# Optimization experiments

Hardware: AMD Instinct MI355X
Metric: run time of the kernel (lower is better)

## Reference

```python
import jax, jax.numpy as jnp
import numpy as np

D_MODEL = 2048
N_HEADS = 16
HEAD_DIM = D_MODEL // N_HEADS  # 128


def setup_inputs() -> dict:
    key = jax.random.key(0)
    ks = jax.random.split(key, 7)
    B, S, CACHE = 2, 2048, 2048
    scale = 1.0 / np.sqrt(D_MODEL)
    return {
        "x": jax.random.normal(ks[0], (B, S, D_MODEL), dtype=jnp.float32),
        "cached_k": jax.random.normal(ks[1], (B, N_HEADS, CACHE, HEAD_DIM), dtype=jnp.float32),
        "cached_v": jax.random.normal(ks[2], (B, N_HEADS, CACHE, HEAD_DIM), dtype=jnp.float32),
        "W_q": jax.random.normal(ks[3], (D_MODEL, D_MODEL), dtype=jnp.float32) * scale,
        "W_k": jax.random.normal(ks[4], (D_MODEL, D_MODEL), dtype=jnp.float32) * scale,
        "W_v": jax.random.normal(ks[5], (D_MODEL, D_MODEL), dtype=jnp.float32) * scale,
        "W_o": jax.random.normal(ks[6], (D_MODEL, D_MODEL), dtype=jnp.float32) * scale,
    }


def reference(x, cached_k, cached_v, W_q, W_k, W_v, W_o):
    B, S, _ = x.shape
    # nn.Linear(d,d,bias=False): y = x @ W.T
    def proj(W):
        h = jnp.einsum("bsd,ed->bse", x, W)
        return h.reshape(B, S, N_HEADS, HEAD_DIM).transpose(0, 2, 1, 3)  # (B,H,S,Dh)
    q = proj(W_q)
    k = jnp.concatenate([cached_k, proj(W_k)], axis=2)  # (B,H,T,Dh)
    v = jnp.concatenate([cached_v, proj(W_v)], axis=2)
    scores = jnp.einsum("bhsd,bhtd->bhst", q, k) / np.sqrt(HEAD_DIM)
    attn = jax.nn.softmax(scores, axis=-1)
    out = jnp.einsum("bhst,bhtd->bhsd", attn, v)  # (B,H,S,Dh)
    out = out.transpose(0, 2, 1, 3).reshape(B, S, D_MODEL)
    out = jnp.einsum("bsd,ed->bse", out, W_o)
    return out, k, v
```

## Files before the change

### kernel.cpp

```cpp
#include <hip/hip_runtime.h>

typedef __bf16 bf16;
typedef __bf16 bf16x4 __attribute__((ext_vector_type(4)));
typedef __bf16 bf16x8 __attribute__((ext_vector_type(8)));
typedef float f32x4 __attribute__((ext_vector_type(4)));

#define LOG2E 1.44269504088896340736f
#define QSCALE 0.12751884935f
#define RESCALE_THR 8.0f

__device__ __forceinline__ void gload_lds16(const void* gp, void* lp) {
    __builtin_amdgcn_global_load_lds(
        (__attribute__((address_space(1))) void*)gp,
        (__attribute__((address_space(3))) void*)lp,
        16, 0, 0);
}

__device__ __forceinline__ int swz(int j, int row) {
    return (j & 8) | ((j ^ row) & 7);
}

template <int CTRL>
__device__ __forceinline__ float dpp_mov(float x) {
    return __int_as_float(__builtin_amdgcn_update_dpp(
        0, __float_as_int(x), CTRL, 0xF, 0xF, true));
}
__device__ __forceinline__ float rowmax16(float v) {
    v = fmaxf(v, dpp_mov<0x121>(v));
    v = fmaxf(v, dpp_mov<0x122>(v));
    v = fmaxf(v, dpp_mov<0x124>(v));
    v = fmaxf(v, dpp_mov<0x128>(v));
    return v;
}
__device__ __forceinline__ float rowsum16(float v) {
    v += dpp_mov<0x121>(v);
    v += dpp_mov<0x122>(v);
    v += dpp_mov<0x124>(v);
    v += dpp_mov<0x128>(v);
    return v;
}

__global__ void conv_bf16(const float* __restrict__ in, bf16* __restrict__ out, int n4) {
    int i = blockIdx.x * 256 + threadIdx.x;
    if (i < n4) {
        float4 f = ((const float4*)in)[i];
        bf16x4 v;
        v[0] = (bf16)f.x; v[1] = (bf16)f.y; v[2] = (bf16)f.z; v[3] = (bf16)f.w;
        *(bf16x4*)(out + (size_t)i * 4) = v;
    }
}

__global__ void copy_cache_k(const float* __restrict__ ck, float* __restrict__ kout,
                             bf16* __restrict__ kb) {
    size_t i = ((size_t)blockIdx.x * 256 + threadIdx.x) * 4;
    size_t bh  = i >> 18;
    size_t rem = i & 262143;
    size_t o   = (bh << 19) + rem;
    float4 f = *(const float4*)(ck + i);
    *(float4*)(kout + o) = f;
    bf16x4 v;
    v[0] = (bf16)f.x; v[1] = (bf16)f.y; v[2] = (bf16)f.z; v[3] = (bf16)f.w;
    *(bf16x4*)(kb + o) = v;
}

__global__ void copy_cache_v(const float* __restrict__ cv, float* __restrict__ vout,
                             bf16* __restrict__ vtb) {
    __shared__ float tile[32][33];
    int bh = blockIdx.z;
    int t0 = blockIdx.x * 32;
    int dh0 = blockIdx.y * 32;
    int tx = threadIdx.x, ty = threadIdx.y;
    const float* src = cv + (size_t)bh * 2048 * 128;
    float* dstf = vout + (size_t)bh * 4096 * 128;
    #pragma unroll
    for (int i = 0; i < 4; ++i) {
        int t = t0 + ty * 4 + i;
        float val = src[(size_t)t * 128 + dh0 + tx];
        dstf[(size_t)t * 128 + dh0 + tx] = val;
        tile[ty * 4 + i][tx] = val;
    }
    __syncthreads();
    bf16* dstb = vtb + (size_t)bh * 128 * 4096;
    #pragma unroll
    for (int i = 0; i < 4; ++i) {
        int dh = dh0 + ty * 4 + i;
        dstb[(size_t)dh * 4096 + t0 + tx] = (bf16)tile[tx][ty * 4 + i];
    }
}

template <int MODE>
__global__ __launch_bounds__(256)
void gemm_nt(const bf16* __restrict__ A, const bf16* __restrict__ Bm,
             float* __restrict__ out_f32, bf16* __restrict__ out_bf16) {
    const int K = 2048, N = 2048;
    __shared__ __align__(16) char smem[32768];
    const int tid = threadIdx.x;
    const int wid = tid >> 6;
    const int lane = tid & 63;
    const int quad = lane >> 4;
    const int l16 = lane & 15;
    const int m0 = blockIdx.y * 128;
    const int n0 = blockIdx.x * 128;
    const int wm = (wid & 1) * 64;
    const int wn = (wid >> 1) * 64;

    f32x4 zero = {0.f, 0.f, 0.f, 0.f};
    f32x4 acc[4][4];
    #pragma unroll
    for (int i = 0; i < 4; ++i)
        #pragma unroll
        for (int j = 0; j < 4; ++j) acc[i][j] = zero;

    auto stage = [&](int k0, int buf) {
        char* base = smem + buf * 16384;
        #pragma unroll
        for (int t = 0; t < 2; ++t) {
            int c = t * 256 + tid;
            int row = c >> 2, kc = c & 3;
            const char* gA = (const char*)(A + (size_t)(m0 + row) * K + k0 + kc * 8);
            const char* gB = (const char*)(Bm + (size_t)(n0 + row) * K + k0 + kc * 8);
            char* lA = base + (size_t)(t * 256 + (tid & ~63)) * 16;
            char* lB = base + 8192 + (size_t)(t * 256 + (tid & ~63)) * 16;
            gload_lds16(gA, lA);
            gload_lds16(gB, lB);
        }
    };

    stage(0, 0);
    __syncthreads();

    for (int k0 = 0; k0 < K; k0 += 32) {
        const int cur = (k0 >> 5) & 1;
        if (k0 + 32 < K) stage(k0 + 32, cur ^ 1);
        const char* base = smem + cur * 16384;
        bf16x8 af[4], bfv[4];
        #pragma unroll
        for (int i = 0; i < 4; ++i) {
            af[i]  = *(const bf16x8*)(base + ((wm + i * 16 + l16) * 32 + quad * 8) * 2);
            bfv[i] = *(const bf16x8*)(base + 8192 + ((wn + i * 16 + l16) * 32 + quad * 8) * 2);
        }
        __builtin_amdgcn_s_setprio(1);
        #pragma unroll
        for (int i = 0; i < 4; ++i)
            #pragma unroll
            for (int j = 0; j < 4; ++j)
                acc[i][j] = __builtin_amdgcn_mfma_f32_16x16x32_bf16(af[i], bfv[j], acc[i][j], 0, 0, 0);
        __builtin_amdgcn_s_setprio(0);
        __syncthreads();
    }

    #pragma unroll
    for (int i = 0; i < 4; ++i)
        #pragma unroll
        for (int j = 0; j < 4; ++j)
            #pragma unroll
            for (int r = 0; r < 4; ++r) {
                int grow = m0 + wm + i * 16 + quad * 4 + r;
                int gcol = n0 + wn + j * 16 + l16;
                float v = acc[i][j][r];
                if (MODE == 0) {
                    out_f32[(size_t)grow * N + gcol] = v;
                } else {
                    int b = grow >> 11, s = grow & 2047;
                    int h = gcol >> 7, dh = gcol & 127;
                    if (MODE == 1) {
                        out_bf16[(((size_t)(b * 16 + h) * 2048) + s) * 128 + dh] = (bf16)(v * QSCALE);
                    } else if (MODE == 2) {
                        size_t idx = (((size_t)(b * 16 + h) * 4096) + 2048 + s) * 128 + dh;
                        out_f32[idx] = v;
                        out_bf16[idx] = (bf16)v;
                    } else {
                        size_t idx = (((size_t)(b * 16 + h) * 4096) + 2048 + s) * 128 + dh;
                        out_f32[idx] = v;
                        out_bf16[(((size_t)(b * 16 + h) * 128) + dh) * 4096 + 2048 + s] = (bf16)v;
                    }
                }
            }
}

__global__ __launch_bounds__(256, 2)
void flash_attn(const bf16* __restrict__ qb, const bf16* __restrict__ kb,
                const bf16* __restrict__ vtb, bf16* __restrict__ ab) {
    __shared__ __align__(16) char smem[74240];
    const int tid = threadIdx.x;
    const int wid = tid >> 6;
    const int lane = tid & 63;
    const int quad = lane >> 4;
    const int l16 = lane & 15;

    const int flat = blockIdx.x;
    const int xcd = flat & 7;
    const int idx = flat >> 3;
    const int bh = xcd * 4 + (idx >> 4);
    const int qblk = idx & 15;
    const int b = bh >> 4, h = bh & 15;
    const int s0 = qblk * 128 + wid * 32;

    const bf16* Q  = qb  + (size_t)bh * 2048 * 128;
    const bf16* Kp = kb  + (size_t)bh * 4096 * 128;
    const bf16* Vt = vtb + (size_t)bh * 128 * 4096;

    bf16x8 qf[2][4];
    #pragma unroll
    for (int qi = 0; qi < 2; ++qi)
        #pragma unroll
        for (int ks = 0; ks < 4; ++ks)
            qf[qi][ks] = *(const bf16x8*)(Q + (size_t)(s0 + qi * 16 + l16) * 128 + ks * 32 + quad * 8);

    f32x4 zero = {0.f, 0.f, 0.f, 0.f};
    f32x4 oacc[2][8];
    float mrun[2][4], lrun[2][4];
    #pragma unroll
    for (int qi = 0; qi < 2; ++qi) {
        #pragma unroll
        for (int i = 0; i < 8; ++i) oacc[qi][i] = zero;
        #pragma unroll
        for (int r = 0; r < 4; ++r) { mrun[qi][r] = -1e30f; lrun[qi][r] = 0.f; }
    }

    auto stage = [&](int t0, int buf) {
        char* Kb = smem + buf * 32768;
        char* Vb = Kb + 16384;
        #pragma unroll
        for (int r = 0; r < 4; ++r) {
            int kc = r * 256 + tid;
            int row = kc >> 4, p = kc & 15;
            int j = swz(p, row);
            gload_lds16(Kp + (size_t)(t0 + row) * 128 + j * 8, Kb + kc * 16);
        }
        #pragma unroll
        for (int r = 0; r < 4; ++r) {
            int vc = r * 256 + tid;
            int row = vc >> 3, p = vc & 7;
            int j = (p ^ row) & 7;
            gload_lds16(Vt + (size_t)row * 4096 + t0 + j * 8, Vb + vc * 16);
        }
    };

    stage(0, 0);
    __syncthreads();

    for (int t0 = 0; t0 < 4096; t0 += 64) {
        const int cur = (t0 >> 6) & 1;
        if (t0 + 64 < 4096) stage(t0 + 64, cur ^ 1);
        const char* Ksh = smem + cur * 32768;
        const char* Vsh = Ksh + 16384;

        f32x4 sacc[2][4];
        #pragma unroll
        for (int qi = 0; qi < 2; ++qi)
            #pragma unroll
            for (int nt = 0; nt < 4; ++nt) sacc[qi][nt] = zero;
        __builtin_amdgcn_s_setprio(1);
        #pragma unroll
        for (int nt = 0; nt < 4; ++nt) {
            #pragma unroll
            for (int ks = 0; ks < 4; ++ks) {
                bf16x8 kf = *(const bf16x8*)(Ksh + (nt * 16 + l16) * 256 + swz(ks * 4 + quad, l16) * 16);
                sacc[0][nt] = __builtin_amdgcn_mfma_f32_16x16x32_bf16(qf[0][ks], kf, sacc[0][nt], 0, 0, 0);
                sacc[1][nt] = __builtin_amdgcn_mfma_f32_16x16x32_bf16(qf[1][ks], kf, sacc[1][nt], 0, 0, 0);
            }
        }
        __builtin_amdgcn_s_setprio(0);

        bf16x8 pf[2][2];
        char* pb = smem + 65536 + wid * 2176;
        #pragma unroll
        for (int qi = 0; qi < 2; ++qi) {
            float mx[4];
            #pragma unroll
            for (int r = 0; r < 4; ++r) {
                float v0 = fmaxf(fmaxf(sacc[qi][0][r], sacc[qi][1][r]),
                                 fmaxf(sacc[qi][2][r], sacc[qi][3][r]));
                mx[r] = rowmax16(v0);
            }
            bool defer = true;
            #pragma unroll
            for (int r = 0; r < 4; ++r)
                defer = defer && (mx[r] <= mrun[qi][r] + RESCALE_THR);
            if (__all(defer)) {
                float rsum[4] = {0.f, 0.f, 0.f, 0.f};
                #pragma unroll
                for (int nt = 0; nt < 4; ++nt)
                    #pragma unroll
                    for (int r = 0; r < 4; ++r) {
                        float p = __builtin_amdgcn_exp2f(sacc[qi][nt][r] - mrun[qi][r]);
                        sacc[qi][nt][r] = p;
                        rsum[r] += p;
                    }
                #pragma unroll
                for (int r = 0; r < 4; ++r) lrun[qi][r] += rowsum16(rsum[r]);
            } else {
                float alpha[4], mnew[4], rsum[4];
                #pragma unroll
                for (int r = 0; r < 4; ++r) {
                    mnew[r] = fmaxf(mrun[qi][r], mx[r]);
                    alpha[r] = __builtin_amdgcn_exp2f(mrun[qi][r] - mnew[r]);
                    rsum[r] = 0.f;
                }
                #pragma unroll
                for (int nt = 0; nt < 4; ++nt)
                    #pragma unroll
                    for (int r = 0; r < 4; ++r) {
                        float p = __builtin_amdgcn_exp2f(sacc[qi][nt][r] - mnew[r]);
                        sacc[qi][nt][r] = p;
                        rsum[r] += p;
                    }
                #pragma unroll
                for (int r = 0; r < 4; ++r) {
                    lrun[qi][r] = lrun[qi][r] * alpha[r] + rowsum16(rsum[r]);
                    mrun[qi][r] = mnew[r];
                }
                #pragma unroll
                for (int i = 0; i < 8; ++i)
                    #pragma unroll
                    for (int r = 0; r < 4; ++r) oacc[qi][i][r] *= alpha[r];
            }

            #pragma unroll
            for (int nt = 0; nt < 4; ++nt)
                #pragma unroll
                for (int r = 0; r < 4; ++r) {
                    int row = quad * 4 + r;
                    *(bf16*)(pb + row * 136 + nt * 32 + l16 * 2) = (bf16)sacc[qi][nt][r];
                }
            #pragma unroll
            for (int ks = 0; ks < 2; ++ks)
                pf[qi][ks] = *(const bf16x8*)(pb + l16 * 136 + (ks * 4 + quad) * 16);
        }

        __builtin_amdgcn_s_setprio(1);
        #pragma unroll
        for (int dht = 0; dht < 8; ++dht) {
            #pragma unroll
            for (int ks = 0; ks < 2; ++ks) {
                bf16x8 vf = *(const bf16x8*)(Vsh + (dht * 16 + l16) * 128 + swz(ks * 4 + quad, l16) * 16);
                oacc[0][dht] = __builtin_amdgcn_mfma_f32_16x16x32_bf16(pf[0][ks], vf, oacc[0][dht], 0, 0, 0);
                oacc[1][dht] = __builtin_amdgcn_mfma_f32_16x16x32_bf16(pf[1][ks], vf, oacc[1][dht], 0, 0, 0);
            }
        }
        __builtin_amdgcn_s_setprio(0);

        __syncthreads();
    }

    #pragma unroll
    for (int qi = 0; qi < 2; ++qi)
        #pragma unroll
        for (int dht = 0; dht < 8; ++dht)
            #pragma unroll
            for (int r = 0; r < 4; ++r) {
                int s = s0 + qi * 16 + quad * 4 + r;
                float v = oacc[qi][dht][r] / lrun[qi][r];
                ab[((size_t)(b * 2048 + s)) * 2048 + h * 128 + dht * 16 + l16] = (bf16)v;
            }
}

extern "C" void kernel_launch(void* const* d_in, const int* in_sizes, int n_in,
                              void* d_out, int out_size, void* d_ws, size_t ws_size,
                              hipStream_t stream) {
    const float* x        = (const float*)d_in[0];
    const float* cached_k = (const float*)d_in[1];
    const float* cached_v = (const float*)d_in[2];
    const float* W_q      = (const float*)d_in[3];
    const float* W_k      = (const float*)d_in[4];
    const float* W_v      = (const float*)d_in[5];
    const float* W_o      = (const float*)d_in[6];

    float* out  = (float*)d_out;
    float* kout = out + 8388608;
    float* vout = out + 25165824;

    char* ws = (char*)d_ws;
    size_t off = 0;
    auto alloc = [&](size_t elts) { bf16* p = (bf16*)(ws + off); off += elts * 2; return p; };
    bf16* xb  = alloc(8388608);
    bf16* wqb = alloc(4194304);
    bf16* wkb = alloc(4194304);
    bf16* wvb = alloc(4194304);
    bf16* wob = alloc(4194304);
    bf16* qb  = alloc(8388608);
    bf16* kb  = alloc(16777216);
    bf16* vtb = alloc(16777216);
    bf16* ab  = alloc(8388608);

    conv_bf16<<<8192, 256, 0, stream>>>(x, xb, 2097152);
    conv_bf16<<<4096, 256, 0, stream>>>(W_q, wqb, 1048576);
    conv_bf16<<<4096, 256, 0, stream>>>(W_k, wkb, 1048576);
    conv_bf16<<<4096, 256, 0, stream>>>(W_v, wvb, 1048576);
    conv_bf16<<<4096, 256, 0, stream>>>(W_o, wob, 1048576);
    copy_cache_k<<<8192, 256, 0, stream>>>(cached_k, kout, kb);
    copy_cache_v<<<dim3(64, 4, 32), dim3(32, 8), 0, stream>>>(cached_v, vout, vtb);

    gemm_nt<1><<<dim3(16, 32), 256, 0, stream>>>(xb, wqb, nullptr, qb);
    gemm_nt<2><<<dim3(16, 32), 256, 0, stream>>>(xb, wkb, kout, kb);
    gemm_nt<3><<<dim3(16, 32), 256, 0, stream>>>(xb, wvb, vout, vtb);

    flash_attn<<<512, 256, 0, stream>>>(qb, kb, vtb, ab);

    gemm_nt<0><<<dim3(16, 32), 256, 0, stream>>>(ab, wob, out, nullptr);
}
```

Baseline: 733.0 us.

## Restructure flash attention to transposed 32x32x16 MFMA with register-resident P

```diff
diff --git a/kernel.cpp b/kernel.cpp
--- a/kernel.cpp
+++ b/kernel.cpp
@@ -4,6 +4,8 @@
 typedef __bf16 bf16x4 __attribute__((ext_vector_type(4)));
 typedef __bf16 bf16x8 __attribute__((ext_vector_type(8)));
 typedef float f32x4 __attribute__((ext_vector_type(4)));
+typedef float f32x16 __attribute__((ext_vector_type(16)));
+typedef int iv2 __attribute__((ext_vector_type(2)));
 
 #define LOG2E 1.44269504088896340736f
 #define QSCALE 0.12751884935f
@@ -20,24 +22,38 @@
     return (j & 8) | ((j ^ row) & 7);
 }
 
-template <int CTRL>
-__device__ __forceinline__ float dpp_mov(float x) {
-    return __int_as_float(__builtin_amdgcn_update_dpp(
-        0, __float_as_int(x), CTRL, 0xF, 0xF, true));
-}
-__device__ __forceinline__ float rowmax16(float v) {
-    v = fmaxf(v, dpp_mov<0x121>(v));
-    v = fmaxf(v, dpp_mov<0x122>(v));
-    v = fmaxf(v, dpp_mov<0x124>(v));
-    v = fmaxf(v, dpp_mov<0x128>(v));
-    return v;
-}
-__device__ __forceinline__ float rowsum16(float v) {
-    v += dpp_mov<0x121>(v);
-    v += dpp_mov<0x122>(v);
-    v += dpp_mov<0x124>(v);
-    v += dpp_mov<0x128>(v);
-    return v;
+__device__ __forceinline__ unsigned cvtpk(float lo, float hi) {
+    unsigned w;
+    asm("v_cvt_pk_bf16_f32 %0, %1, %2" : "=v"(w) : "v"(lo), "v"(hi));
+    return w;
+}
+
+__device__ __forceinline__ iv2 permswap(unsigned a, unsigned b) {
+    return __builtin_amdgcn_permlane32_swap((int)a, (int)b, false, false);
+}
+__device__ __forceinline__ float halfmax(float v) {
+    iv2 r = permswap(__float_as_uint(v), __float_as_uint(v));
+    return fmaxf(__int_as_float(r[0]), __int_as_float(r[1]));
+}
+__device__ __forceinline__ float halfadd(float v) {
+    iv2 r = permswap(__float_as_uint(v), __float_as_uint(v));
+    return __int_as_float(r[0]) + __int_as_float(r[1]);
+}
+
+__device__ __forceinline__ float vmax32(const f32x16& a, const f32x16& b) {
+    float t[8];
+    #pragma unroll
+    for (int i = 0; i < 8; ++i)
+        t[i] = fmaxf(fmaxf(a[i], a[i + 8]), fmaxf(b[i], b[i + 8]));
+    return fmaxf(fmaxf(fmaxf(t[0], t[1]), fmaxf(t[2], t[3])),
+                 fmaxf(fmaxf(t[4], t[5]), fmaxf(t[6], t[7])));
+}
+__device__ __forceinline__ float vsum32(const f32x16& a, const f32x16& b) {
+    float t[8];
+    #pragma unroll
+    for (int i = 0; i < 8; ++i)
+        t[i] = (a[i] + a[i + 8]) + (b[i] + b[i + 8]);
+    return ((t[0] + t[1]) + (t[2] + t[3])) + ((t[4] + t[5]) + (t[6] + t[7]));
 }
 
 __global__ void conv_bf16(const float* __restrict__ in, bf16* __restrict__ out, int n4) {
@@ -181,12 +197,12 @@
 __global__ __launch_bounds__(256, 2)
 void flash_attn(const bf16* __restrict__ qb, const bf16* __restrict__ kb,
                 const bf16* __restrict__ vtb, bf16* __restrict__ ab) {
-    __shared__ __align__(16) char smem[74240];
+    __shared__ __align__(16) char smem[65536];
     const int tid = threadIdx.x;
     const int wid = tid >> 6;
     const int lane = tid & 63;
-    const int quad = lane >> 4;
-    const int l16 = lane & 15;
+    const int hh = lane >> 5;
+    const int l31 = lane & 31;
 
     const int flat = blockIdx.x;
     const int xcd = flat & 7;
@@ -200,23 +216,17 @@
     const bf16* Kp = kb  + (size_t)bh * 4096 * 128;
     const bf16* Vt = vtb + (size_t)bh * 128 * 4096;
 
-    bf16x8 qf[2][4];
-    #pragma unroll
-    for (int qi = 0; qi < 2; ++qi)
-        #pragma unroll
-        for (int ks = 0; ks < 4; ++ks)
-            qf[qi][ks] = *(const bf16x8*)(Q + (size_t)(s0 + qi * 16 + l16) * 128 + ks * 32 + quad * 8);
-
-    f32x4 zero = {0.f, 0.f, 0.f, 0.f};
-    f32x4 oacc[2][8];
-    float mrun[2][4], lrun[2][4];
-    #pragma unroll
-    for (int qi = 0; qi < 2; ++qi) {
-        #pragma unroll
-        for (int i = 0; i < 8; ++i) oacc[qi][i] = zero;
-        #pragma unroll
-        for (int r = 0; r < 4; ++r) { mrun[qi][r] = -1e30f; lrun[qi][r] = 0.f; }
-    }
+    bf16x8 qf[8];
+    #pragma unroll
+    for (int ks = 0; ks < 8; ++ks)
+        qf[ks] = *(const bf16x8*)(Q + (size_t)(s0 + l31) * 128 + ks * 16 + hh * 8);
+
+    f32x16 oacc[4];
+    #pragma unroll
+    for (int dhb = 0; dhb < 4; ++dhb)
+        #pragma unroll
+        for (int i = 0; i < 16; ++i) oacc[dhb][i] = 0.f;
+    float mrun = -1e30f, lrun = 0.f;
 
     auto stage = [&](int t0, int buf) {
         char* Kb = smem + buf * 32768;
@@ -246,114 +256,82 @@
         const char* Ksh = smem + cur * 32768;
         const char* Vsh = Ksh + 16384;
 
-        f32x4 sacc[2][4];
-        #pragma unroll
-        for (int qi = 0; qi < 2; ++qi)
-            #pragma unroll
-            for (int nt = 0; nt < 4; ++nt) sacc[qi][nt] = zero;
+        f32x16 sacc[2];
+        #pragma unroll
+        for (int i = 0; i < 16; ++i) { sacc[0][i] = 0.f; sacc[1][i] = 0.f; }
         __builtin_amdgcn_s_setprio(1);
         #pragma unroll
-        for (int nt = 0; nt < 4; ++nt) {
+        for (int ks = 0; ks < 8; ++ks) {
+            const int r0 = l31, r1 = 32 + l31;
+            bf16x8 kf0 = *(const bf16x8*)(Ksh + r0 * 256 + swz(ks * 2 + hh, r0) * 16);
+            bf16x8 kf1 = *(const bf16x8*)(Ksh + r1 * 256 + swz(ks * 2 + hh, r1) * 16);
+            sacc[0] = __builtin_amdgcn_mfma_f32_32x32x16_bf16(kf0, qf[ks], sacc[0], 0, 0, 0);
+            sacc[1] = __builtin_amdgcn_mfma_f32_32x32x16_bf16(kf1, qf[ks], sacc[1], 0, 0, 0);
+        }
+        __builtin_amdgcn_s_setprio(0);
+
+        float mx = halfmax(vmax32(sacc[0], sacc[1]));
+        if (!__all(mx <= mrun + RESCALE_THR)) {
+            float mnew = fmaxf(mrun, mx);
+            float alpha = __builtin_amdgcn_exp2f(mrun - mnew);
+            #pragma unroll
+            for (int dhb = 0; dhb < 4; ++dhb)
+                #pragma unroll
+                for (int i = 0; i < 16; ++i) oacc[dhb][i] *= alpha;
+            lrun *= alpha;
+            mrun = mnew;
+        }
+        #pragma unroll
+        for (int tb = 0; tb < 2; ++tb)
+            #pragma unroll
+            for (int i = 0; i < 16; ++i)
+                sacc[tb][i] = __builtin_amdgcn_exp2f(sacc[tb][i] - mrun);
+        lrun += halfadd(vsum32(sacc[0], sacc[1]));
+
+        bf16x8 pf[4];
+        #pragma unroll
+        for (int tb = 0; tb < 2; ++tb)
+            #pragma unroll
+            for (int ksl = 0; ksl < 2; ++ksl) {
+                const int g0 = ksl * 8;
+                unsigned wa0 = cvtpk(sacc[tb][g0 + 0], sacc[tb][g0 + 1]);
+                unsigned wb0 = cvtpk(sacc[tb][g0 + 4], sacc[tb][g0 + 5]);
+                unsigned wa1 = cvtpk(sacc[tb][g0 + 2], sacc[tb][g0 + 3]);
+                unsigned wb1 = cvtpk(sacc[tb][g0 + 6], sacc[tb][g0 + 7]);
+                iv2 r0 = permswap(wa0, wb0);
+                iv2 r1 = permswap(wa1, wb1);
+                union { int u[4]; bf16x8 v; } pk;
+                pk.u[0] = r0[0]; pk.u[1] = r1[0]; pk.u[2] = r0[1]; pk.u[3] = r1[1];
+                pf[tb * 2 + ksl] = pk.v;
+            }
+
+        __builtin_amdgcn_s_setprio(1);
+        #pragma unroll
+        for (int dhb = 0; dhb < 4; ++dhb) {
+            const int row = dhb * 32 + l31;
             #pragma unroll
             for (int ks = 0; ks < 4; ++ks) {
-                bf16x8 kf = *(const bf16x8*)(Ksh + (nt * 16 + l16) * 256 + swz(ks * 4 + quad, l16) * 16);
-                sacc[0][nt] = __builtin_amdgcn_mfma_f32_16x16x32_bf16(qf[0][ks], kf, sacc[0][nt], 0, 0, 0);
-                sacc[1][nt] = __builtin_amdgcn_mfma_f32_16x16x32_bf16(qf[1][ks], kf, sacc[1][nt], 0, 0, 0);
+                bf16x8 vf = *(const bf16x8*)(Vsh + row * 128 + (((ks * 2 + hh) ^ row) & 7) * 16);
+                oacc[dhb] = __builtin_amdgcn_mfma_f32_32x32x16_bf16(vf, pf[ks], oacc[dhb], 0, 0, 0);
             }
         }
         __builtin_amdgcn_s_setprio(0);
 
-        bf16x8 pf[2][2];
-        char* pb = smem + 65536 + wid * 2176;
-        #pragma unroll
-        for (int qi = 0; qi < 2; ++qi) {
-            float mx[4];
-            #pragma unroll
-            for (int r = 0; r < 4; ++r) {
-                float v0 = fmaxf(fmaxf(sacc[qi][0][r], sacc[qi][1][r]),
-                                 fmaxf(sacc[qi][2][r], sacc[qi][3][r]));
-                mx[r] = rowmax16(v0);
-            }
-            bool defer = true;
-            #pragma unroll
-            for (int r = 0; r < 4; ++r)
-                defer = defer && (mx[r] <= mrun[qi][r] + RESCALE_THR);
-            if (__all(defer)) {
-                float rsum[4] = {0.f, 0.f, 0.f, 0.f};
-                #pragma unroll
-                for (int nt = 0; nt < 4; ++nt)
-                    #pragma unroll
-                    for (int r = 0; r < 4; ++r) {
-                        float p = __builtin_amdgcn_exp2f(sacc[qi][nt][r] - mrun[qi][r]);
-                        sacc[qi][nt][r] = p;
-                        rsum[r] += p;
-                    }
-                #pragma unroll
-                for (int r = 0; r < 4; ++r) lrun[qi][r] += rowsum16(rsum[r]);
-            } else {
-                float alpha[4], mnew[4], rsum[4];
-                #pragma unroll
-                for (int r = 0; r < 4; ++r) {
-                    mnew[r] = fmaxf(mrun[qi][r], mx[r]);
-                    alpha[r] = __builtin_amdgcn_exp2f(mrun[qi][r] - mnew[r]);
-                    rsum[r] = 0.f;
-                }
-                #pragma unroll
-                for (int nt = 0; nt < 4; ++nt)
-                    #pragma unroll
-                    for (int r = 0; r < 4; ++r) {
-                        float p = __builtin_amdgcn_exp2f(sacc[qi][nt][r] - mnew[r]);
-                        sacc[qi][nt][r] = p;
-                        rsum[r] += p;
-                    }
-                #pragma unroll
-                for (int r = 0; r < 4; ++r) {
-                    lrun[qi][r] = lrun[qi][r] * alpha[r] + rowsum16(rsum[r]);
-                    mrun[qi][r] = mnew[r];
-                }
-                #pragma unroll
-                for (int i = 0; i < 8; ++i)
-                    #pragma unroll
-                    for (int r = 0; r < 4; ++r) oacc[qi][i][r] *= alpha[r];
-            }
-
-            #pragma unroll
-            for (int nt = 0; nt < 4; ++nt)
-                #pragma unroll
-                for (int r = 0; r < 4; ++r) {
-                    int row = quad * 4 + r;
-                    *(bf16*)(pb + row * 136 + nt * 32 + l16 * 2) = (bf16)sacc[qi][nt][r];
-                }
-            #pragma unroll
-            for (int ks = 0; ks < 2; ++ks)
-                pf[qi][ks] = *(const bf16x8*)(pb + l16 * 136 + (ks * 4 + quad) * 16);
-        }
-
-        __builtin_amdgcn_s_setprio(1);
-        #pragma unroll
-        for (int dht = 0; dht < 8; ++dht) {
-            #pragma unroll
-            for (int ks = 0; ks < 2; ++ks) {
-                bf16x8 vf = *(const bf16x8*)(Vsh + (dht * 16 + l16) * 128 + swz(ks * 4 + quad, l16) * 16);
-                oacc[0][dht] = __builtin_amdgcn_mfma_f32_16x16x32_bf16(pf[0][ks], vf, oacc[0][dht], 0, 0, 0);
-                oacc[1][dht] = __builtin_amdgcn_mfma_f32_16x16x32_bf16(pf[1][ks], vf, oacc[1][dht], 0, 0, 0);
-            }
-        }
-        __builtin_amdgcn_s_setprio(0);
-
         __syncthreads();
     }
 
-    #pragma unroll
-    for (int qi = 0; qi < 2; ++qi)
-        #pragma unroll
-        for (int dht = 0; dht < 8; ++dht)
-            #pragma unroll
-            for (int r = 0; r < 4; ++r) {
-                int s = s0 + qi * 16 + quad * 4 + r;
-                float v = oacc[qi][dht][r] / lrun[qi][r];
-                ab[((size_t)(b * 2048 + s)) * 2048 + h * 128 + dht * 16 + l16] = (bf16)v;
-            }
+    const float inv = 1.0f / lrun;
+    const int s = s0 + l31;
+    #pragma unroll
+    for (int dhb = 0; dhb < 4; ++dhb)
+        #pragma unroll
+        for (int g = 0; g < 4; ++g) {
+            bf16x4 o4;
+            #pragma unroll
+            for (int r = 0; r < 4; ++r) o4[r] = (bf16)(oacc[dhb][g * 4 + r] * inv);
+            int dh = dhb * 32 + g * 8 + hh * 4;
+            *(bf16x4*)(ab + ((size_t)(b * 2048 + s)) * 2048 + h * 128 + dh) = o4;
+        }
 }
 
 extern "C" void kernel_launch(void* const* d_in, const int* in_sizes, int n_in,
```

Result: faster. 655.0 us (-10.6%).
